# Optimization experiments

Measured on AMD Instinct MI355X. Metric: run time of the kernel, lower is better.

## Reference

```python
import jax, jax.numpy as jnp
import numpy as np

# Clos factorization for in=out=4096, middle_switch_multiplier=4:
BIN, B1, B2, B3, BOUT = 64, 64, 256, 64, 64
B, C, D = 2, 4096, 4096


def setup_inputs() -> dict:
    key = jax.random.key(0)
    ks = jax.random.split(key, 7)
    k = 1.0 / np.sqrt(D)
    x = jax.random.normal(ks[0], (B, C, D), dtype=jnp.float32)
    # kaiming_uniform(a=sqrt(5)) on [bin,b1,b2]-like tensors ~ uniform(-bound, bound)
    w1 = jax.random.uniform(ks[1], (BIN, B1, B2), jnp.float32, -k, k)
    w2 = jax.random.uniform(ks[2], (B1, B2, B3), jnp.float32, -k, k)
    w3 = jax.random.uniform(ks[3], (B2, B3, BOUT), jnp.float32, -k, k)
    bias1 = jax.random.uniform(ks[4], (B1,), jnp.float32, -k, k)
    bias2 = jax.random.uniform(ks[5], (B2,), jnp.float32, -k, k)
    bias3 = jax.random.uniform(ks[6], (B3,), jnp.float32, -k, k)
    return {"x": x, "w1": w1, "w2": w2, "w3": w3,
            "bias1": bias1, "bias2": bias2, "bias3": bias3}


def reference(x, w1, w2, w3, bias1, bias2, bias3):
    b, c, _ = x.shape
    h = x.reshape(b, c, BIN, B1)                      # [b,c,n=bin,r=b1]
    h = jnp.einsum('bcnr,nrm->bcmr', h, w1) + bias1   # [b,c,b2,b1] + bias over b1
    h = jnp.einsum('bcmr,rmn->bcnm', h, w2) + bias2   # [b,c,b3,b2] + bias over b2
    h = jnp.einsum('bcnm,mro->bcor', h, w3) + bias3   # [b,c,bout,b3] + bias over b3
    return h.reshape(b, c, -1)                        # [b,c,out_features]
```

## Files before the change

### kernel.cpp

```cpp
#include <hip/hip_runtime.h>
#include <stdint.h>
#include <stddef.h>

typedef __bf16 bf16_t;
typedef __bf16 bf16x8 __attribute__((ext_vector_type(8)));
typedef __bf16 bf16x4 __attribute__((ext_vector_type(4)));
typedef float f32x4 __attribute__((ext_vector_type(4)));

__device__ __forceinline__ void gload_lds16(const void* g, void* l) {
  __builtin_amdgcn_global_load_lds(
      (const __attribute__((address_space(1))) uint32_t*)g,
      (__attribute__((address_space(3))) uint32_t*)l, 16, 0, 0);
}

__global__ void prep1_k(const float* __restrict__ w2, const float* __restrict__ w3,
                        float* __restrict__ w2s, bf16_t* __restrict__ w3pt) {
  __shared__ float lds[64][65];
  const int b = blockIdx.x;
  const int t = threadIdx.x;
  if (b < 64) {
    const int r = b, m = t;
    const float4* p = (const float4*)(w2 + ((size_t)(r * 256 + m)) * 64);
    float s = 0.f;
#pragma unroll
    for (int i = 0; i < 16; ++i) {
      float4 v = p[i];
      s += (v.x + v.y) + (v.z + v.w);
    }
    w2s[r * 256 + m] = s;
    return;
  }
  const int b2 = b - 64;
  const int r = b2 & 63;
  const int mt = (b2 >> 6) * 64;
#pragma unroll
  for (int it = 0; it < 16; ++it) {
    int idx = t + it * 256;
    int ml = idx >> 6, o = idx & 63;
    lds[ml][o] = w3[(size_t)(mt + ml) * 4096 + r * 64 + o];
  }
  __syncthreads();
#pragma unroll
  for (int it = 0; it < 16; ++it) {
    int idx = t + it * 256;
    int o = idx >> 6, ml = idx & 63;
    w3pt[(size_t)(o * 64 + r) * 256 + mt + ml] = (bf16_t)lds[ml][o];
  }
}

__global__ void prep2_k(const float* __restrict__ w1, const float* __restrict__ w2s,
                        const float* __restrict__ bias1, const float* __restrict__ bias2,
                        bf16_t* __restrict__ w1t, float* __restrict__ c2) {
  __shared__ float lds[64][65];
  const int b = blockIdx.x;
  const int t = threadIdx.x;
  if (b == 256) {
    float s = 64.f * bias2[t];
#pragma unroll 8
    for (int r = 0; r < 64; ++r) s += bias1[r] * w2s[r * 256 + t];
    c2[t] = s;
    return;
  }
  const int k0 = (b >> 2) * 64;
  const int mt = (b & 3) * 64;
#pragma unroll
  for (int it = 0; it < 16; ++it) {
    int idx = t + it * 256;
    int kl = idx >> 6, ml = idx & 63;
    int k = k0 + kl;
    lds[kl][ml] = w1[(size_t)k * 256 + mt + ml] * w2s[(k & 63) * 256 + mt + ml];
  }
  __syncthreads();
#pragma unroll
  for (int it = 0; it < 16; ++it) {
    int idx = t + it * 256;
    int ml = idx >> 6, kl = idx & 63;
    w1t[(size_t)(mt + ml) * 4096 + k0 + kl] = (bf16_t)lds[kl][ml];
  }
}

__global__ __launch_bounds__(512, 1) void gemm1_k(
    const float* __restrict__ X, const bf16_t* __restrict__ W1T,
    const float* __restrict__ c2, bf16_t* __restrict__ S) {
  __shared__ __align__(16) bf16_t lA[2][64 * 64];
  __shared__ __align__(16) bf16_t lB[2][256 * 64];
  const int tid = threadIdx.x;
  const int lane = tid & 63;
  const int wv = tid >> 6;
  const int mtile = (int)blockIdx.x >> 1;
  const int kh = (int)blockIdx.x & 1;
  const size_t m0 = (size_t)mtile * 64;
  const int kbase = kh * 2048;
  const int wm = wv >> 2, wn = wv & 3;
  const int r0 = tid >> 4;
  const int f4 = tid & 15;

  f32x4 acc[2][4];
#pragma unroll
  for (int i = 0; i < 2; ++i)
#pragma unroll
    for (int j = 0; j < 4; ++j) acc[i][j] = (f32x4){0.f, 0.f, 0.f, 0.f};

  float4 aReg[2];

  auto issueA = [&](int kt) {
#pragma unroll
    for (int p = 0; p < 2; ++p) {
      int row = r0 + p * 32;
      aReg[p] = *(const float4*)(X + (m0 + row) * 4096 + (size_t)(kbase + kt * 64 + f4 * 4));
    }
  };
  auto writeA = [&](int buf) {
#pragma unroll
    for (int p = 0; p < 2; ++p) {
      int row = r0 + p * 32;
      int off = row * 128 + ((f4 * 8) ^ ((row & 7) << 4));
      bf16x4 v;
      v[0] = (bf16_t)aReg[p].x;
      v[1] = (bf16_t)aReg[p].y;
      v[2] = (bf16_t)aReg[p].z;
      v[3] = (bf16_t)aReg[p].w;
      *(bf16x4*)((char*)(&lA[buf][0]) + off) = v;
    }
  };
  auto issueB = [&](int buf, int kt) {
#pragma unroll
    for (int i = 0; i < 4; ++i) {
      int row = wv * 32 + i * 8 + (lane >> 3);
      int srckb = ((lane & 7) * 16) ^ ((row & 7) << 4);
      const char* src = (const char*)W1T + (size_t)row * 8192 + (size_t)(kbase + kt * 64) * 2 + srckb;
      char* dst = (char*)(&lB[buf][0]) + (wv * 32 + i * 8) * 128;
      gload_lds16(src, dst);
    }
  };
  auto compute = [&](int buf) {
#pragma unroll
    for (int kk = 0; kk < 2; ++kk) {
      const int kb = kk * 64 + ((lane >> 4) * 16);
      bf16x8 af[2], bfr[4];
#pragma unroll
      for (int mf = 0; mf < 2; ++mf) {
        int row = wm * 32 + mf * 16 + (lane & 15);
        int off = row * 128 + (kb ^ ((row & 7) << 4));
        af[mf] = *(const bf16x8*)((const char*)(&lA[buf][0]) + off);
      }
#pragma unroll
      for (int nf = 0; nf < 4; ++nf) {
        int row = wn * 64 + nf * 16 + (lane & 15);
        int off = row * 128 + (kb ^ ((row & 7) << 4));
        bfr[nf] = *(const bf16x8*)((const char*)(&lB[buf][0]) + off);
      }
#pragma unroll
      for (int mf = 0; mf < 2; ++mf)
#pragma unroll
        for (int nf = 0; nf < 4; ++nf)
          acc[mf][nf] = __builtin_amdgcn_mfma_f32_16x16x32_bf16(af[mf], bfr[nf], acc[mf][nf], 0, 0, 0);
    }
  };

  issueA(0);
  issueB(0, 0);
  writeA(0);
  __syncthreads();
#pragma unroll 1
  for (int kt = 0; kt < 32; ++kt) {
    int cur = kt & 1;
    bool more = (kt + 1) < 32;
    if (more) {
      issueA(kt + 1);
      issueB(cur ^ 1, kt + 1);
    }
    compute(cur);
    if (more) writeA(cur ^ 1);
    __syncthreads();
  }

#pragma unroll
  for (int nf = 0; nf < 4; ++nf) {
    int col = wn * 64 + nf * 16 + (lane & 15);
    float cadd = (kh == 0) ? c2[col] : 0.f;
#pragma unroll
    for (int mf = 0; mf < 2; ++mf) {
#pragma unroll
      for (int q = 0; q < 4; ++q) {
        int row = wm * 32 + mf * 16 + (lane >> 4) * 4 + q;
        S[(m0 + row) * 512 + (size_t)(kh * 256 + col)] = (bf16_t)(acc[mf][nf][q] + cadd);
      }
    }
  }
}

__global__ __launch_bounds__(256, 1) void gemm2_k(
    const bf16_t* __restrict__ S, const bf16_t* __restrict__ W3pT,
    const float* __restrict__ bias3, float* __restrict__ OUT) {
  __shared__ __align__(16) bf16_t lA[2][128 * 64];
  __shared__ __align__(16) bf16_t lB[2][128 * 64];
  const int tid = threadIdx.x;
  const int lane = tid & 63;
  const int wv = tid >> 6;
  const int mt = (int)blockIdx.x >> 5;
  const int nt = (int)blockIdx.x & 31;
  const size_t m0 = (size_t)mt * 128;
  const int n0 = nt * 128;
  const int wm = wv >> 1, wn = wv & 1;

  f32x4 acc[4][4];
#pragma unroll
  for (int i = 0; i < 4; ++i)
#pragma unroll
    for (int j = 0; j < 4; ++j) acc[i][j] = (f32x4){0.f, 0.f, 0.f, 0.f};

  auto stage = [&](int buf, int kt) {
#pragma unroll
    for (int i = 0; i < 4; ++i) {
      int row = wv * 32 + i * 8 + (lane >> 3);
      int srckb = ((lane & 7) * 16) ^ ((row & 7) << 4);
      const char* srcA = (const char*)S + (m0 + row) * 1024 + (size_t)(kt * 128 + srckb);
      char* dstA = (char*)(&lA[buf][0]) + (wv * 32 + i * 8) * 128;
      gload_lds16(srcA, dstA);
      const char* srcB = (const char*)W3pT + (size_t)(n0 + row) * 512 + (size_t)((kt & 3) * 128 + srckb);
      char* dstB = (char*)(&lB[buf][0]) + (wv * 32 + i * 8) * 128;
      gload_lds16(srcB, dstB);
    }
  };
  auto compute = [&](int buf) {
#pragma unroll
    for (int kk = 0; kk < 2; ++kk) {
      const int kb = kk * 64 + ((lane >> 4) * 16);
      bf16x8 af[4], bfr[4];
#pragma unroll
      for (int mf = 0; mf < 4; ++mf) {
        int row = wm * 64 + mf * 16 + (lane & 15);
        int off = row * 128 + (kb ^ ((row & 7) << 4));
        af[mf] = *(const bf16x8*)((const char*)(&lA[buf][0]) + off);
      }
#pragma unroll
      for (int nf = 0; nf < 4; ++nf) {
        int row = wn * 64 + nf * 16 + (lane & 15);
        int off = row * 128 + (kb ^ ((row & 7) << 4));
        bfr[nf] = *(const bf16x8*)((const char*)(&lB[buf][0]) + off);
      }
#pragma unroll
      for (int mf = 0; mf < 4; ++mf)
#pragma unroll
        for (int nf = 0; nf < 4; ++nf)
          acc[mf][nf] = __builtin_amdgcn_mfma_f32_16x16x32_bf16(af[mf], bfr[nf], acc[mf][nf], 0, 0, 0);
    }
  };

  stage(0, 0);
  __syncthreads();
#pragma unroll 1
  for (int kt = 0; kt < 8; ++kt) {
    int cur = kt & 1;
    if (kt + 1 < 8) stage(cur ^ 1, kt + 1);
    compute(cur);
    __syncthreads();
  }

#pragma unroll
  for (int nf = 0; nf < 4; ++nf) {
    int jcol = wn * 64 + nf * 16 + (lane & 15);
    float b3 = bias3[jcol & 63];
    int j = n0 + jcol;
#pragma unroll
    for (int mf = 0; mf < 4; ++mf) {
#pragma unroll
      for (int q = 0; q < 4; ++q) {
        size_t row = m0 + (size_t)(wm * 64 + mf * 16 + (lane >> 4) * 4 + q);
        OUT[row * 4096 + j] = acc[mf][nf][q] + b3;
      }
    }
  }
}

extern "C" void kernel_launch(void* const* d_in, const int* in_sizes, int n_in,
                              void* d_out, int out_size, void* d_ws, size_t ws_size,
                              hipStream_t stream) {
  (void)in_sizes; (void)n_in; (void)out_size; (void)ws_size;
  const float* x  = (const float*)d_in[0];
  const float* w1 = (const float*)d_in[1];
  const float* w2 = (const float*)d_in[2];
  const float* w3 = (const float*)d_in[3];
  const float* b1 = (const float*)d_in[4];
  const float* b2 = (const float*)d_in[5];
  const float* b3 = (const float*)d_in[6];
  float* out = (float*)d_out;
  char* ws = (char*)d_ws;

  float*  w2s  = (float*)(ws + 0);
  float*  c2   = (float*)(ws + 65536);
  bf16_t* w1t  = (bf16_t*)(ws + 69632);
  bf16_t* w3pt = (bf16_t*)(ws + 69632 + 2097152);
  bf16_t* S    = (bf16_t*)(ws + 69632 + 2 * 2097152);

  prep1_k<<<320, 256, 0, stream>>>(w2, w3, w2s, w3pt);
  prep2_k<<<257, 256, 0, stream>>>(w1, w2s, b1, b2, w1t, c2);
  gemm1_k<<<256, 512, 0, stream>>>(x, w1t, c2, S);
  gemm2_k<<<2048, 256, 0, stream>>>(S, w3pt, b3, out);
}
```

Before: 120.1 us.

## Split gemm1 K four ways, add reduce kernel, and halve gemm2 K

gemm1 now splits K four ways across 512 blocks, writing bf16 partial sums into a wider scratch buffer. A new reduce kernel sums the four partials, adds c2, and produces a compact 256-wide S. gemm2 therefore runs K=256 instead of folding the split halves over K=512, and switches to 8 waves with a 4x2 fragment layout. The aim is better CU occupancy in gemm1 and half the MFMA work in gemm2. The cost is an extra launch, roughly 16MB more scratch traffic, and extra bf16 rounding of the partials.

New measurement: 103.5 us. 1.16x faster.

```diff
diff --git a/kernel.cpp b/kernel.cpp
--- a/kernel.cpp
+++ b/kernel.cpp
@@ -81,16 +81,16 @@
 
 __global__ __launch_bounds__(512, 1) void gemm1_k(
     const float* __restrict__ X, const bf16_t* __restrict__ W1T,
-    const float* __restrict__ c2, bf16_t* __restrict__ S) {
+    bf16_t* __restrict__ S4) {
   __shared__ __align__(16) bf16_t lA[2][64 * 64];
   __shared__ __align__(16) bf16_t lB[2][256 * 64];
   const int tid = threadIdx.x;
   const int lane = tid & 63;
   const int wv = tid >> 6;
-  const int mtile = (int)blockIdx.x >> 1;
-  const int kh = (int)blockIdx.x & 1;
+  const int mtile = (int)blockIdx.x >> 2;
+  const int kh = (int)blockIdx.x & 3;
   const size_t m0 = (size_t)mtile * 64;
-  const int kbase = kh * 2048;
+  const int kbase = kh * 1024;
   const int wm = wv >> 2, wn = wv & 3;
   const int r0 = tid >> 4;
   const int f4 = tid & 15;
@@ -163,9 +163,9 @@
   writeA(0);
   __syncthreads();
 #pragma unroll 1
-  for (int kt = 0; kt < 32; ++kt) {
+  for (int kt = 0; kt < 16; ++kt) {
     int cur = kt & 1;
-    bool more = (kt + 1) < 32;
+    bool more = (kt + 1) < 16;
     if (more) {
       issueA(kt + 1);
       issueB(cur ^ 1, kt + 1);
@@ -178,19 +178,40 @@
 #pragma unroll
   for (int nf = 0; nf < 4; ++nf) {
     int col = wn * 64 + nf * 16 + (lane & 15);
-    float cadd = (kh == 0) ? c2[col] : 0.f;
 #pragma unroll
     for (int mf = 0; mf < 2; ++mf) {
 #pragma unroll
       for (int q = 0; q < 4; ++q) {
         int row = wm * 32 + mf * 16 + (lane >> 4) * 4 + q;
-        S[(m0 + row) * 512 + (size_t)(kh * 256 + col)] = (bf16_t)(acc[mf][nf][q] + cadd);
-      }
-    }
-  }
-}
-
-__global__ __launch_bounds__(256, 1) void gemm2_k(
+        S4[(m0 + row) * 1024 + (size_t)(kh * 256 + col)] = (bf16_t)acc[mf][nf][q];
+      }
+    }
+  }
+}
+
+__global__ void reduce_k(const bf16_t* __restrict__ S4, const float* __restrict__ c2,
+                         bf16_t* __restrict__ S) {
+  int gid = blockIdx.x * 256 + threadIdx.x;
+  int row = gid >> 5;
+  int c8 = (gid & 31) << 3;
+  float s[8];
+  float4 ca = *(const float4*)(c2 + c8);
+  float4 cb = *(const float4*)(c2 + c8 + 4);
+  s[0] = ca.x; s[1] = ca.y; s[2] = ca.z; s[3] = ca.w;
+  s[4] = cb.x; s[5] = cb.y; s[6] = cb.z; s[7] = cb.w;
+#pragma unroll
+  for (int h = 0; h < 4; ++h) {
+    bf16x8 v = *(const bf16x8*)(S4 + (size_t)row * 1024 + h * 256 + c8);
+#pragma unroll
+    for (int j = 0; j < 8; ++j) s[j] += (float)v[j];
+  }
+  bf16x8 o;
+#pragma unroll
+  for (int j = 0; j < 8; ++j) o[j] = (bf16_t)s[j];
+  *(bf16x8*)(S + (size_t)row * 256 + c8) = o;
+}
+
+__global__ __launch_bounds__(512, 1) void gemm2_k(
     const bf16_t* __restrict__ S, const bf16_t* __restrict__ W3pT,
     const float* __restrict__ bias3, float* __restrict__ OUT) {
   __shared__ __align__(16) bf16_t lA[2][128 * 64];
@@ -202,24 +223,24 @@
   const int nt = (int)blockIdx.x & 31;
   const size_t m0 = (size_t)mt * 128;
   const int n0 = nt * 128;
-  const int wm = wv >> 1, wn = wv & 1;
-
-  f32x4 acc[4][4];
+  const int wm = wv >> 2, wn = wv & 3;
+
+  f32x4 acc[4][2];
 #pragma unroll
   for (int i = 0; i < 4; ++i)
 #pragma unroll
-    for (int j = 0; j < 4; ++j) acc[i][j] = (f32x4){0.f, 0.f, 0.f, 0.f};
+    for (int j = 0; j < 2; ++j) acc[i][j] = (f32x4){0.f, 0.f, 0.f, 0.f};
 
   auto stage = [&](int buf, int kt) {
 #pragma unroll
-    for (int i = 0; i < 4; ++i) {
-      int row = wv * 32 + i * 8 + (lane >> 3);
+    for (int p = 0; p < 2; ++p) {
+      int row = wv * 8 + (lane >> 3) + p * 64;
       int srckb = ((lane & 7) * 16) ^ ((row & 7) << 4);
-      const char* srcA = (const char*)S + (m0 + row) * 1024 + (size_t)(kt * 128 + srckb);
-      char* dstA = (char*)(&lA[buf][0]) + (wv * 32 + i * 8) * 128;
+      const char* srcA = (const char*)S + (m0 + row) * 512 + (size_t)(kt * 128 + srckb);
+      char* dstA = (char*)(&lA[buf][0]) + (wv * 8 + p * 64) * 128;
       gload_lds16(srcA, dstA);
-      const char* srcB = (const char*)W3pT + (size_t)(n0 + row) * 512 + (size_t)((kt & 3) * 128 + srckb);
-      char* dstB = (char*)(&lB[buf][0]) + (wv * 32 + i * 8) * 128;
+      const char* srcB = (const char*)W3pT + (size_t)(n0 + row) * 512 + (size_t)(kt * 128 + srckb);
+      char* dstB = (char*)(&lB[buf][0]) + (wv * 8 + p * 64) * 128;
       gload_lds16(srcB, dstB);
     }
   };
@@ -227,7 +248,7 @@
 #pragma unroll
     for (int kk = 0; kk < 2; ++kk) {
       const int kb = kk * 64 + ((lane >> 4) * 16);
-      bf16x8 af[4], bfr[4];
+      bf16x8 af[4], bfr[2];
 #pragma unroll
       for (int mf = 0; mf < 4; ++mf) {
         int row = wm * 64 + mf * 16 + (lane & 15);
@@ -235,15 +256,15 @@
         af[mf] = *(const bf16x8*)((const char*)(&lA[buf][0]) + off);
       }
 #pragma unroll
-      for (int nf = 0; nf < 4; ++nf) {
-        int row = wn * 64 + nf * 16 + (lane & 15);
+      for (int nf = 0; nf < 2; ++nf) {
+        int row = wn * 32 + nf * 16 + (lane & 15);
         int off = row * 128 + (kb ^ ((row & 7) << 4));
         bfr[nf] = *(const bf16x8*)((const char*)(&lB[buf][0]) + off);
       }
 #pragma unroll
       for (int mf = 0; mf < 4; ++mf)
 #pragma unroll
-        for (int nf = 0; nf < 4; ++nf)
+        for (int nf = 0; nf < 2; ++nf)
           acc[mf][nf] = __builtin_amdgcn_mfma_f32_16x16x32_bf16(af[mf], bfr[nf], acc[mf][nf], 0, 0, 0);
     }
   };
@@ -251,16 +272,16 @@
   stage(0, 0);
   __syncthreads();
 #pragma unroll 1
-  for (int kt = 0; kt < 8; ++kt) {
+  for (int kt = 0; kt < 4; ++kt) {
     int cur = kt & 1;
-    if (kt + 1 < 8) stage(cur ^ 1, kt + 1);
+    if (kt + 1 < 4) stage(cur ^ 1, kt + 1);
     compute(cur);
     __syncthreads();
   }
 
 #pragma unroll
-  for (int nf = 0; nf < 4; ++nf) {
-    int jcol = wn * 64 + nf * 16 + (lane & 15);
+  for (int nf = 0; nf < 2; ++nf) {
+    int jcol = wn * 32 + nf * 16 + (lane & 15);
     float b3 = bias3[jcol & 63];
     int j = n0 + jcol;
 #pragma unroll
@@ -292,10 +313,12 @@
   float*  c2   = (float*)(ws + 65536);
   bf16_t* w1t  = (bf16_t*)(ws + 69632);
   bf16_t* w3pt = (bf16_t*)(ws + 69632 + 2097152);
-  bf16_t* S    = (bf16_t*)(ws + 69632 + 2 * 2097152);
+  bf16_t* S4   = (bf16_t*)(ws + 69632 + 2 * 2097152);
+  bf16_t* S    = (bf16_t*)(ws + 69632 + 2 * 2097152 + 16777216);
 
   prep1_k<<<320, 256, 0, stream>>>(w2, w3, w2s, w3pt);
   prep2_k<<<257, 256, 0, stream>>>(w1, w2s, b1, b2, w1t, c2);
-  gemm1_k<<<256, 512, 0, stream>>>(x, w1t, c2, S);
-  gemm2_k<<<2048, 256, 0, stream>>>(S, w3pt, b3, out);
-}
+  gemm1_k<<<512, 512, 0, stream>>>(x, w1t, S4);
+  reduce_k<<<1024, 256, 0, stream>>>(S4, c2, S);
+  gemm2_k<<<2048, 512, 0, stream>>>(S, w3pt, b3, out);
+}
```
